# Optimization experiments

Measured on AMD Instinct MI355X. Metric: run time of the kernel, lower is better.

The kernel has to match this reference:

```python
import jax, jax.numpy as jnp
import numpy as np

B, F0, D = 4096, 39, 16
CROSS_LAYER_SIZE = (128, 128)


def _he_uniform(key, shape):
    fan_in = int(np.prod(shape[:-1]))
    limit = np.sqrt(6.0 / fan_in)
    return jax.random.uniform(key, shape, jnp.float32, -limit, limit)


def setup_inputs() -> dict:
    key = jax.random.key(0)
    k_x, k_f0, k_f1, k_w, k_b = jax.random.split(key, 5)
    x = jax.random.normal(k_x, (B, F0, D), dtype=jnp.float32)
    # field_nums with direct=False: [39, 128//2=64, 64]
    f0 = _he_uniform(k_f0, (F0 * F0, CROSS_LAYER_SIZE[0]))          # (1521, 128)
    f1 = _he_uniform(k_f1, (F0 * (CROSS_LAYER_SIZE[0] // 2), CROSS_LAYER_SIZE[1]))  # (2496, 128)
    out_dim = CROSS_LAYER_SIZE[0] // 2 + CROSS_LAYER_SIZE[1]        # 192
    dense_w = _he_uniform(k_w, (out_dim, 1))
    dense_b = jnp.zeros((1,), dtype=jnp.float32)
    return {"x": x, "f0": f0, "f1": f1, "dense_w": dense_w, "dense_b": dense_b}


def reference(x, f0, f1, dense_w, dense_b):
    # CIN forward (direct=False, use_bias=False, use_residual=False, relu)
    # x: (B, F0, D)
    filters = [f0, f1]
    n_layers = len(CROSS_LAYER_SIZE)
    h = x  # hidden state, (B, Fk, D)
    finals = []
    for idx, L in enumerate(CROSS_LAYER_SIZE):
        Fk = h.shape[1]
        # filter f_ has shape (F0*Fk, L) with i (field of x0) major, j (field of h) minor
        Wr = filters[idx].reshape(F0, Fk, L)
        # fused outer product + conv1d (kernel width 1 == matmul over i,j):
        # z[b, m, d] = sum_{i,j} x[b,i,d] * h[b,j,d] * W[i,j,m]
        z = jnp.einsum('bid,bjd,ijm->bmd', x, h, Wr)  # (B, L, D)
        z = jax.nn.relu(z)
        if idx != n_layers - 1:
            # split along feature-map axis: first half feeds next layer,
            # second half goes to output
            h = z[:, : L // 2, :]
            finals.append(z[:, L // 2:, :])
        else:
            finals.append(z)
    result = jnp.sum(jnp.concatenate(finals, axis=1), axis=-1)  # (B, 192)
    return result @ dense_w + dense_b  # (B, 1)
```

## Files before the change

### kernel.cpp

```cpp
#include <hip/hip_runtime.h>


typedef _Float16 h2    __attribute__((ext_vector_type(2)));
typedef _Float16 f16x8 __attribute__((ext_vector_type(8)));
typedef __attribute__((ext_vector_type(16))) float f32x16;

#define XBB 1160
#define L0C 30
#define NCH 110

__device__ __constant__ int IG0[L0C] = {0,0,0,0,0, 1,1,1,1,1, 2,2,2,2, 3,3,3,3, 4,4,4, 5,5,5, 6,6, 7,7, 8, 9};
__device__ __constant__ int JG0[L0C] = {0,1,2,3,4, 0,1,2,3,4, 1,2,3,4, 1,2,3,4, 2,3,4, 2,3,4, 3,4, 3,4, 4, 4};
#define IG0T(c) ((c)<5?0:(c)<10?1:(c)<14?2:(c)<18?3:(c)<21?4:(c)<24?5:(c)<26?6:(c)<28?7:(c)<29?8:9)
#define JG0T(c) ((c)<10?((c)%5):(c)<18?(((c)-10)%4+1):(c)<24?(((c)-18)%3+2):(c)<28?(((c)-24)%2+3):4)

__global__ __launch_bounds__(256)
void CIN_repack(const float* __restrict__ f0, const float* __restrict__ f1,
                uint4* __restrict__ ws)
{
    const int tid  = blockIdx.x * 256 + threadIdx.x;
    const int n    = tid & 127;
    const int slot = tid >> 7;
    const int half = slot & 1;
    const int kh   = (slot >> 1) & 1;
    const int ch   = slot >> 2;
    float v[8];
    if (ch < L0C) {
        const int ig = IG0[ch], jg = JG0[ch];
        const int i = ig * 4 + kh * 2 + half;
#pragma unroll
        for (int t = 0; t < 8; ++t) {
            const int j = jg * 8 + t;
            float val = 0.f;
            if (i < 39 && j < 39 && j >= i) {
                val = f0[(i * 39 + j) * 128 + n];
                if (j > i) val += f0[(j * 39 + i) * 128 + n];
            }
            v[t] = val;
        }
    } else {
        const int c1 = ch - L0C;
        const int jg = c1 / 5, ig = c1 - jg * 5;
        const int j = jg * 4 + kh * 2 + half;
#pragma unroll
        for (int t = 0; t < 8; ++t) {
            const int i = ig * 8 + t;
            v[t] = (i < 39) ? f1[(i * 64 + j) * 128 + n] : 0.f;
        }
    }
    union { h2 h[4]; uint4 q; } pk;
#pragma unroll
    for (int t = 0; t < 4; ++t)
        pk.h[t] = h2{(_Float16)v[2 * t], (_Float16)v[2 * t + 1]};
    const int lane = half * 32 + (n & 31);
    const int cg   = n >> 5;
    ws[ch * 512 + kh * 256 + cg * 64 + lane] = pk.q;
}

__global__ __launch_bounds__(256, 2)
void CIN_main(const float* __restrict__ x,
              const char* __restrict__ wsB,
              const float* __restrict__ dw,
              const float* __restrict__ db,
              float* __restrict__ out)
{
    __shared__ __align__(16) _Float16 xsH[4 * XBB];
    __shared__ __align__(4)  _Float16 hsH[4][64][18];
    __shared__ float dws[192];
    __shared__ float red[4][4];

    const int tid  = threadIdx.x;
    const int w    = tid >> 6;
    const int lane = tid & 63;
    const int half = lane >> 5;
    const int d    = lane & 15;
    const int bsel = (lane >> 4) & 1;
    const int col  = lane & 31;

    const char* wbase = wsB + lane * 16 + w * 1024 + 2048;
    f16x8 Bb[4][2];
    auto loadBg = [&](int ch, f16x8 (&B)[2]) {
        const char* p0 = wbase + (size_t)ch * 8192;
        B[0] = *(const f16x8*)(p0 - 2048);
        B[1] = *(const f16x8*)(p0 + 2048);
    };

    loadBg(0, Bb[0]);
    loadBg(1, Bb[1]);
    loadBg(2, Bb[2]);
    loadBg(3, Bb[3]);

    const float4* xg4 = (const float4*)(x + (size_t)blockIdx.x * 4 * 624);
    for (int e4 = tid; e4 < 624; e4 += 256) {
        float4 v = xg4[e4];
        int bb = e4 / 156, r = e4 - bb * 156;
        int i = r >> 2, d0 = (r & 3) * 4;
        _Float16* bp = xsH + bb * XBB + i;
        bp[(d0 + 0) * 72] = (_Float16)v.x; bp[(d0 + 1) * 72] = (_Float16)v.y;
        bp[(d0 + 2) * 72] = (_Float16)v.z; bp[(d0 + 3) * 72] = (_Float16)v.w;
    }
    if (tid < 64) { int bb = tid >> 4, dd = tid & 15; xsH[bb * XBB + dd * 72 + 39] = (_Float16)0.f; }
    if (tid < 192) dws[tid] = dw[tid];
    __syncthreads();

    const _Float16* xrow[2] = {
        xsH + (0 * 2 + bsel) * XBB + d * 72,
        xsH + (1 * 2 + bsel) * XBB + d * 72
    };

    h2 xw[2][20];
#pragma unroll
    for (int p = 0; p < 2; ++p)
#pragma unroll
        for (int w5 = 0; w5 < 5; ++w5) {
            union { f16x8 v; h2 h[4]; } u;
            u.v = *(const f16x8*)(xrow[p] + w5 * 8);
#pragma unroll
            for (int q = 0; q < 4; ++q) xw[p][w5 * 4 + q] = u.h[q];
        }

    f32x16 acc[2];
#pragma unroll
    for (int p = 0; p < 2; ++p)
#pragma unroll
        for (int r = 0; r < 16; ++r) acc[p][r] = 0.f;

    h2 sp2[2][2];

#pragma unroll
    for (int c = 0; c < L0C; ++c) {
        const int ig = IG0T(c);
        const int jg = JG0T(c);
        if ((c == 0) || (IG0T(c) != IG0T(c - 1))) {
#pragma unroll
            for (int p = 0; p < 2; ++p)
#pragma unroll
                for (int kh = 0; kh < 2; ++kh) {
                    const h2 pr = xw[p][ig * 2 + kh];
                    const _Float16 vv = half ? pr.y : pr.x;
                    sp2[p][kh] = h2{vv, vv};
                }
        }
#pragma unroll
        for (int p = 0; p < 2; ++p) {
            union { h2 h[4]; f16x8 v; } a0, a1;
#pragma unroll
            for (int q = 0; q < 4; ++q) {
                a0.h[q] = sp2[p][0] * xw[p][jg * 4 + q];
                a1.h[q] = sp2[p][1] * xw[p][jg * 4 + q];
            }
            acc[p] = __builtin_amdgcn_mfma_f32_32x32x16_f16(a0.v, Bb[c & 3][0], acc[p], 0, 0, 0);
            acc[p] = __builtin_amdgcn_mfma_f32_32x32x16_f16(a1.v, Bb[c & 3][1], acc[p], 0, 0, 0);
        }
        loadBg(c + 4, Bb[c & 3]);
    }

    float cs[4] = {0.f, 0.f, 0.f, 0.f};
    if (w < 2) {
#pragma unroll
        for (int p = 0; p < 2; ++p)
#pragma unroll
            for (int r = 0; r < 16; r += 2) {
                const int row = (r & 3) + 8 * (r >> 2) + 4 * half;
                h2 pr = h2{(_Float16)fmaxf(acc[p][r],     0.f),
                           (_Float16)fmaxf(acc[p][r + 1], 0.f)};
                *(h2*)&hsH[p * 2 + (row >> 4)][w * 32 + col][row & 15] = pr;
            }
    } else {
        const float dwv = dws[(w - 2) * 32 + col];
#pragma unroll
        for (int p = 0; p < 2; ++p)
#pragma unroll
            for (int r = 0; r < 16; ++r) {
                const int row = (r & 3) + 8 * (r >> 2) + 4 * half;
                cs[p * 2 + (row >> 4)] += fmaxf(acc[p][r], 0.f) * dwv;
            }
    }
#pragma unroll
    for (int p = 0; p < 2; ++p)
#pragma unroll
        for (int r = 0; r < 16; ++r) acc[p][r] = 0.f;
    __syncthreads();

#pragma unroll 1
    for (int o2 = 0; o2 < 4; ++o2) {
#pragma unroll
        for (int u = 0; u < 20; ++u) {
            const int ig2 = u % 5;
            if (ig2 == 0) {
                const int jb = (o2 * 4 + u / 5) * 4;
#pragma unroll
                for (int p = 0; p < 2; ++p)
#pragma unroll
                    for (int kh = 0; kh < 2; ++kh) {
                        const _Float16 s = hsH[p * 2 + bsel][jb + kh * 2 + half][d];
                        sp2[p][kh] = h2{s, s};
                    }
            }
#pragma unroll
            for (int p = 0; p < 2; ++p) {
                union { h2 h[4]; f16x8 v; } a0, a1;
#pragma unroll
                for (int q = 0; q < 4; ++q) {
                    a0.h[q] = sp2[p][0] * xw[p][ig2 * 4 + q];
                    a1.h[q] = sp2[p][1] * xw[p][ig2 * 4 + q];
                }
                acc[p] = __builtin_amdgcn_mfma_f32_32x32x16_f16(a0.v, Bb[(2 + u) & 3][0], acc[p], 0, 0, 0);
                acc[p] = __builtin_amdgcn_mfma_f32_32x32x16_f16(a1.v, Bb[(2 + u) & 3][1], acc[p], 0, 0, 0);
            }
            int chn = 30 + o2 * 20 + u + 4; if (chn > NCH - 1) chn = NCH - 1;
            loadBg(chn, Bb[(2 + u) & 3]);
        }
    }

    {
        const float dwv = dws[64 + w * 32 + col];
#pragma unroll
        for (int p = 0; p < 2; ++p)
#pragma unroll
            for (int r = 0; r < 16; ++r) {
                const int row = (r & 3) + 8 * (r >> 2) + 4 * half;
                cs[p * 2 + (row >> 4)] += fmaxf(acc[p][r], 0.f) * dwv;
            }
    }
#pragma unroll
    for (int rr = 0; rr < 4; ++rr)
#pragma unroll
        for (int off = 32; off > 0; off >>= 1)
            cs[rr] += __shfl_xor(cs[rr], off, 64);
    if (lane == 0) {
#pragma unroll
        for (int rr = 0; rr < 4; ++rr) red[w][rr] = cs[rr];
    }
    __syncthreads();
    if (tid < 4)
        out[blockIdx.x * 4 + tid] = red[0][tid] + red[1][tid] + red[2][tid] + red[3][tid] + db[0];
}

extern "C" void kernel_launch(void* const* d_in, const int* in_sizes, int n_in,
                              void* d_out, int out_size, void* d_ws, size_t ws_size,
                              hipStream_t stream)
{
    const float* x  = (const float*)d_in[0];
    const float* f0 = (const float*)d_in[1];
    const float* f1 = (const float*)d_in[2];
    const float* dw = (const float*)d_in[3];
    const float* db = (const float*)d_in[4];
    float* out = (float*)d_out;

    CIN_repack<<<dim3(220), dim3(256), 0, stream>>>(f0, f1, (uint4*)d_ws);
    CIN_main<<<dim3(1024), dim3(256), 0, stream>>>(x, (const char*)d_ws, dw, db, out);
}
```

Baseline: 123.8 us.

## Fuse weight repack and main CIN kernel via cooperative launch with grid sync

Merges the filter repack kernel and the main CIN kernel into a single cooperative kernel. Each block does its share of the repack and stages x into shared memory, then does a grid-wide sync before the MFMA compute. This removes one kernel launch and overlaps x staging with the repack. In exchange it requires all 1024 blocks to be co-resident (launch bound raised to 4 blocks/CU), which can force register spills, and it adds a grid barrier plus host occupancy queries on every call, with a two-kernel fallback.

```diff
diff --git a/kernel.cpp b/kernel.cpp
--- a/kernel.cpp
+++ b/kernel.cpp
@@ -1,4 +1,7 @@
 #include <hip/hip_runtime.h>
+#include <hip/hip_cooperative_groups.h>
+
+namespace cg = cooperative_groups;
 
 
 typedef _Float16 h2    __attribute__((ext_vector_type(2)));
@@ -14,13 +17,13 @@
 #define IG0T(c) ((c)<5?0:(c)<10?1:(c)<14?2:(c)<18?3:(c)<21?4:(c)<24?5:(c)<26?6:(c)<28?7:(c)<29?8:9)
 #define JG0T(c) ((c)<10?((c)%5):(c)<18?(((c)-10)%4+1):(c)<24?(((c)-18)%3+2):(c)<28?(((c)-24)%2+3):4)
 
-__global__ __launch_bounds__(256)
-void CIN_repack(const float* __restrict__ f0, const float* __restrict__ f1,
-                uint4* __restrict__ ws)
-{
-    const int tid  = blockIdx.x * 256 + threadIdx.x;
-    const int n    = tid & 127;
-    const int slot = tid >> 7;
+static __device__ __forceinline__ void repack_slot(int gtid,
+                                                   const float* __restrict__ f0,
+                                                   const float* __restrict__ f1,
+                                                   uint4* __restrict__ ws)
+{
+    const int n    = gtid & 127;
+    const int slot = gtid >> 7;
     const int half = slot & 1;
     const int kh   = (slot >> 1) & 1;
     const int ch   = slot >> 2;
@@ -57,18 +60,13 @@
     ws[ch * 512 + kh * 256 + cg * 64 + lane] = pk.q;
 }
 
-__global__ __launch_bounds__(256, 2)
-void CIN_main(const float* __restrict__ x,
-              const char* __restrict__ wsB,
-              const float* __restrict__ dw,
-              const float* __restrict__ db,
-              float* __restrict__ out)
-{
-    __shared__ __align__(16) _Float16 xsH[4 * XBB];
-    __shared__ __align__(4)  _Float16 hsH[4][64][18];
-    __shared__ float dws[192];
-    __shared__ float red[4][4];
-
+static __device__ __forceinline__ void main_body(
+    const float* __restrict__ x, const char* __restrict__ wsB,
+    const float* __restrict__ dw, const float* __restrict__ db,
+    float* __restrict__ out,
+    _Float16* xsH, _Float16* hsH , float* dws, float* red ,
+    bool stage_x)
+{
     const int tid  = threadIdx.x;
     const int w    = tid >> 6;
     const int lane = tid & 63;
@@ -77,6 +75,34 @@
     const int bsel = (lane >> 4) & 1;
     const int col  = lane & 31;
 
+    if (stage_x) {
+        const float4* xg4 = (const float4*)(x + (size_t)blockIdx.x * 4 * 624);
+        for (int e4 = tid; e4 < 624; e4 += 256) {
+            float4 v = xg4[e4];
+            int bb = e4 / 156, r = e4 - bb * 156;
+            int i = r >> 2, d0 = (r & 3) * 4;
+            _Float16* bp = xsH + bb * XBB + i;
+            bp[(d0 + 0) * 72] = (_Float16)v.x; bp[(d0 + 1) * 72] = (_Float16)v.y;
+            bp[(d0 + 2) * 72] = (_Float16)v.z; bp[(d0 + 3) * 72] = (_Float16)v.w;
+        }
+        if (tid < 64) { int bb = tid >> 4, dd = tid & 15; xsH[bb * XBB + dd * 72 + 39] = (_Float16)0.f; }
+        if (tid < 192) dws[tid] = dw[tid];
+        __syncthreads();
+    }
+
+    const _Float16* xrow[2] = { xsH + bsel * XBB + d * 72, xsH + (2 + bsel) * XBB + d * 72 };
+
+    h2 xw[2][20];
+#pragma unroll
+    for (int p = 0; p < 2; ++p)
+#pragma unroll
+        for (int w5 = 0; w5 < 5; ++w5) {
+            union { f16x8 v; h2 h[4]; } u;
+            u.v = *(const f16x8*)(xrow[p] + w5 * 8);
+#pragma unroll
+            for (int q = 0; q < 4; ++q) xw[p][w5 * 4 + q] = u.h[q];
+        }
+
     const char* wbase = wsB + lane * 16 + w * 1024 + 2048;
     f16x8 Bb[4][2];
     auto loadBg = [&](int ch, f16x8 (&B)[2]) {
@@ -84,40 +110,7 @@
         B[0] = *(const f16x8*)(p0 - 2048);
         B[1] = *(const f16x8*)(p0 + 2048);
     };
-
-    loadBg(0, Bb[0]);
-    loadBg(1, Bb[1]);
-    loadBg(2, Bb[2]);
-    loadBg(3, Bb[3]);
-
-    const float4* xg4 = (const float4*)(x + (size_t)blockIdx.x * 4 * 624);
-    for (int e4 = tid; e4 < 624; e4 += 256) {
-        float4 v = xg4[e4];
-        int bb = e4 / 156, r = e4 - bb * 156;
-        int i = r >> 2, d0 = (r & 3) * 4;
-        _Float16* bp = xsH + bb * XBB + i;
-        bp[(d0 + 0) * 72] = (_Float16)v.x; bp[(d0 + 1) * 72] = (_Float16)v.y;
-        bp[(d0 + 2) * 72] = (_Float16)v.z; bp[(d0 + 3) * 72] = (_Float16)v.w;
-    }
-    if (tid < 64) { int bb = tid >> 4, dd = tid & 15; xsH[bb * XBB + dd * 72 + 39] = (_Float16)0.f; }
-    if (tid < 192) dws[tid] = dw[tid];
-    __syncthreads();
-
-    const _Float16* xrow[2] = {
-        xsH + (0 * 2 + bsel) * XBB + d * 72,
-        xsH + (1 * 2 + bsel) * XBB + d * 72
-    };
-
-    h2 xw[2][20];
-#pragma unroll
-    for (int p = 0; p < 2; ++p)
-#pragma unroll
-        for (int w5 = 0; w5 < 5; ++w5) {
-            union { f16x8 v; h2 h[4]; } u;
-            u.v = *(const f16x8*)(xrow[p] + w5 * 8);
-#pragma unroll
-            for (int q = 0; q < 4; ++q) xw[p][w5 * 4 + q] = u.h[q];
-        }
+    loadBg(0, Bb[0]); loadBg(1, Bb[1]); loadBg(2, Bb[2]); loadBg(3, Bb[3]);
 
     f32x16 acc[2];
 #pragma unroll
@@ -164,7 +157,7 @@
                 const int row = (r & 3) + 8 * (r >> 2) + 4 * half;
                 h2 pr = h2{(_Float16)fmaxf(acc[p][r],     0.f),
                            (_Float16)fmaxf(acc[p][r + 1], 0.f)};
-                *(h2*)&hsH[p * 2 + (row >> 4)][w * 32 + col][row & 15] = pr;
+                *(h2*)&hsH[(p * 2 + (row >> 4)) * (64 * 18) + (w * 32 + col) * 18 + (row & 15)] = pr;
             }
     } else {
         const float dwv = dws[(w - 2) * 32 + col];
@@ -193,7 +186,8 @@
                 for (int p = 0; p < 2; ++p)
 #pragma unroll
                     for (int kh = 0; kh < 2; ++kh) {
-                        const _Float16 s = hsH[p * 2 + bsel][jb + kh * 2 + half][d];
+                        const _Float16 s =
+                            hsH[(p * 2 + bsel) * (64 * 18) + (jb + kh * 2 + half) * 18 + d];
                         sp2[p][kh] = h2{s, s};
                     }
             }
@@ -230,11 +224,72 @@
             cs[rr] += __shfl_xor(cs[rr], off, 64);
     if (lane == 0) {
 #pragma unroll
-        for (int rr = 0; rr < 4; ++rr) red[w][rr] = cs[rr];
+        for (int rr = 0; rr < 4; ++rr) red[w * 4 + rr] = cs[rr];
     }
     __syncthreads();
     if (tid < 4)
-        out[blockIdx.x * 4 + tid] = red[0][tid] + red[1][tid] + red[2][tid] + red[3][tid] + db[0];
+        out[blockIdx.x * 4 + tid] = red[0 + tid] + red[4 + tid] + red[8 + tid] + red[12 + tid] + db[0];
+}
+
+__global__ __launch_bounds__(256)
+void CIN_repack(const float* __restrict__ f0, const float* __restrict__ f1,
+                uint4* __restrict__ ws)
+{
+    const int gtid = blockIdx.x * 256 + threadIdx.x;
+    if (gtid < 56320) repack_slot(gtid, f0, f1, ws);
+}
+
+__global__ __launch_bounds__(256, 2)
+void CIN_main(const float* __restrict__ x, const char* __restrict__ wsB,
+              const float* __restrict__ dw, const float* __restrict__ db,
+              float* __restrict__ out)
+{
+    __shared__ __align__(16) _Float16 xsH[4 * XBB];
+    __shared__ __align__(4)  _Float16 hsH[4 * 64 * 18];
+    __shared__ float dws[192];
+    __shared__ float red[16];
+    main_body(x, wsB, dw, db, out, xsH, hsH, dws, red, true);
+}
+
+__global__ __launch_bounds__(256, 4)
+void CIN_fused(const float* __restrict__ x,
+               const float* __restrict__ f0,
+               const float* __restrict__ f1,
+               const float* __restrict__ dw,
+               const float* __restrict__ db,
+               uint4* __restrict__ ws,
+               float* __restrict__ out)
+{
+    __shared__ __align__(16) _Float16 xsH[4 * XBB];
+    __shared__ __align__(4)  _Float16 hsH[4 * 64 * 18];
+    __shared__ float dws[192];
+    __shared__ float red[16];
+
+    const int tid  = threadIdx.x;
+    const int gtid = blockIdx.x * 256 + tid;
+
+    if (gtid < 56320) repack_slot(gtid, f0, f1, ws);
+
+    {
+        const float4* xg4 = (const float4*)(x + (size_t)blockIdx.x * 4 * 624);
+        for (int e4 = tid; e4 < 624; e4 += 256) {
+            float4 v = xg4[e4];
+            int bb = e4 / 156, r = e4 - bb * 156;
+            int i = r >> 2, d0 = (r & 3) * 4;
+            _Float16* bp = xsH + bb * XBB + i;
+            bp[(d0 + 0) * 72] = (_Float16)v.x; bp[(d0 + 1) * 72] = (_Float16)v.y;
+            bp[(d0 + 2) * 72] = (_Float16)v.z; bp[(d0 + 3) * 72] = (_Float16)v.w;
+        }
+        if (tid < 64) { int bb = tid >> 4, dd = tid & 15; xsH[bb * XBB + dd * 72 + 39] = (_Float16)0.f; }
+        if (tid < 192) dws[tid] = dw[tid];
+    }
+    __syncthreads();
+
+    __threadfence();
+    cg::this_grid().sync();
+    __threadfence();
+
+    main_body(x, (const char*)ws, dw, db, out, xsH, hsH, dws, red, false);
 }
 
 extern "C" void kernel_launch(void* const* d_in, const int* in_sizes, int n_in,
@@ -247,7 +302,24 @@
     const float* dw = (const float*)d_in[3];
     const float* db = (const float*)d_in[4];
     float* out = (float*)d_out;
-
-    CIN_repack<<<dim3(220), dim3(256), 0, stream>>>(f0, f1, (uint4*)d_ws);
-    CIN_main<<<dim3(1024), dim3(256), 0, stream>>>(x, (const char*)d_ws, dw, db, out);
-}
+    uint4* ws = (uint4*)d_ws;
+
+    int dev = 0;
+    (void)hipGetDevice(&dev);
+    int numCU = 0;
+    (void)hipDeviceGetAttribute(&numCU, hipDeviceAttributeMultiprocessorCount, dev);
+    int maxBlk = 0;
+    hipError_t qe = hipOccupancyMaxActiveBlocksPerMultiprocessor(&maxBlk, CIN_fused, 256, 0);
+
+    hipError_t le = hipErrorUnknown;
+    if (qe == hipSuccess && numCU > 0 && maxBlk * numCU >= 1024) {
+        void* args[] = { (void*)&x, (void*)&f0, (void*)&f1, (void*)&dw,
+                         (void*)&db, (void*)&ws, (void*)&out };
+        le = hipLaunchCooperativeKernel(CIN_fused, dim3(1024), dim3(256),
+                                        args, 0, stream);
+    }
+    if (le != hipSuccess) {
+        CIN_repack<<<dim3(220), dim3(256), 0, stream>>>(f0, f1, ws);
+        CIN_main<<<dim3(1024), dim3(256), 0, stream>>>(x, (const char*)ws, dw, db, out);
+    }
+}
```

New measurement: 126.3 us. 2.0% more time.
